# Performance work log

Measured on AMD Instinct MI355X. Metric: run time of the kernel, lower is better.

The kernel has to match this reference:

```python
import jax, jax.numpy as jnp
import numpy as np

BCE_W, AMP_W, SMOOTH_W = 1.0, 0.5, 0.3
BIG = 1e30  # finite sentinel for masked min/max (avoids inf-inf NaNs)


def setup_inputs() -> dict:
    key = jax.random.key(0)
    k1, k2, k3 = jax.random.split(key, 3)
    B, L = 128, 100000
    signals = jax.random.normal(k1, (B, 1, L), dtype=jnp.float32)
    predictions = jax.random.normal(k2, (B, L, 1), dtype=jnp.float32)
    targets = jax.random.uniform(k3, (B, L, 1), dtype=jnp.float32)
    return {"signals": signals, "predictions": predictions, "targets": targets}


def _window_amp(mask, s, idx, L):
    # mask: [B, L] bool; s: [B, L] signal. Amplitude of s over [min_idx, max_idx].
    lo = jnp.min(jnp.where(mask, idx, L), axis=1)    # [B]
    hi = jnp.max(jnp.where(mask, idx, -1), axis=1)   # [B]
    w = (idx[None, :] >= lo[:, None]) & (idx[None, :] <= hi[:, None])  # [B, L]
    amp = jnp.max(jnp.where(w, s, -BIG), axis=1) - jnp.min(jnp.where(w, s, BIG), axis=1)
    return amp, jnp.any(mask, axis=1)


def reference(signals, predictions, targets):
    # predictions/targets: [B, L, 1] (3D path of the torch module)
    p, t = predictions, targets
    pred_sigmoid = jax.nn.sigmoid(p)
    # BCEWithLogitsLoss (mean), numerically stable
    bce_loss = jnp.mean(jnp.maximum(p, 0.0) - p * t + jnp.log1p(jnp.exp(-jnp.abs(p))))

    B, L = signals.shape[0], signals.shape[2]
    s = signals[:, 0, :]                              # [B, L]
    idx = jnp.arange(L)

    true_amp, t_has = _window_amp(t[:, :, 0] > 0.5, s, idx, L)
    pred_amp, p_has = _window_amp(pred_sigmoid[:, :, 0] > 0.5, s, idx, L)
    valid = t_has & p_has

    d = jnp.abs(true_amp - pred_amp)
    per = jnp.where(true_amp > 1e-6, d / (true_amp + 1e-6), d)
    amp_loss = jnp.sum(jnp.where(valid, per, 0.0)) / B

    # smoothness: mean |diff(pred_sigmoid, axis=1)|; L >= 2 so never empty
    smoothness_loss = jnp.mean(jnp.abs(pred_sigmoid[:, 1:, :] - pred_sigmoid[:, :-1, :]))

    return BCE_W * bce_loss + AMP_W * amp_loss + SMOOTH_W * smoothness_loss
```

## Files before the change

kernel.cpp:

```cpp
#include <hip/hip_runtime.h>
#include <math.h>
#include <float.h>

#define BATCH 128
#define LEN   100000
#define BPR   4
#define CHUNK (LEN / BPR)
#define VPS   (CHUNK / 4)
#define T     1024
#define NFULL 6
#define TAILV (VPS - NFULL * T)
#define NG    (NFULL + 1)
#define NST   NG
#define STRE  (T * 4)
#define TAILE (TAILV * 4)
#define NSEG  (BATCH * BPR)
#define NSTR  (NSEG * NST)

struct WS {
    int*   lt_tab; int* ht_tab; int* lp_tab; int* hp_tab;
    float* bce_blk; float* sm_blk;
    float* cmin; float* cmax;
    float* wmn; float* wmx;
};

static inline WS ws_layout(void* d_ws) {
    WS w;
    w.lt_tab  = (int*)d_ws;
    w.ht_tab  = w.lt_tab + NSEG;
    w.lp_tab  = w.ht_tab + NSEG;
    w.hp_tab  = w.lp_tab + NSEG;
    w.bce_blk = (float*)(w.hp_tab + NSEG);
    w.sm_blk  = w.bce_blk + NSEG;
    w.cmin    = w.sm_blk  + NSEG;
    w.cmax    = w.cmin    + NSTR;
    w.wmn     = w.cmax    + NSTR;
    w.wmx     = w.wmn     + 2 * BATCH;
    return w;
}


__global__ __launch_bounds__(T) void k_main(
        const float* __restrict__ sig,
        const float* __restrict__ pred,
        const float* __restrict__ targ,
        int* __restrict__ lt_tab, int* __restrict__ ht_tab,
        int* __restrict__ lp_tab, int* __restrict__ hp_tab,
        float* __restrict__ bce_blk, float* __restrict__ sm_blk,
        float* __restrict__ cmin_tab, float* __restrict__ cmax_tab) {
    const int b   = blockIdx.y;
    const int blk = blockIdx.x;
    const int tid = threadIdx.x;
    const size_t row = (size_t)b * LEN;
    const float* prow = pred + row;
    const float* trow = targ + row;
    const float* srow = sig  + row;
    const int base = blk * CHUNK;
    const int w = tid >> 6, lane = tid & 63;

    __shared__ float s_stmn[16][NST], s_stmx[16][NST];
    __shared__ float s_bce[16], s_sm[16];
    __shared__ int   s_lt[16], s_ht[16], s_lp[16], s_hp[16];

    float bce = 0.0f, sm = 0.0f;
    unsigned tmask = 0u, pmask = 0u;

    #pragma unroll
    for (int k = 0; k < NG; ++k) {
        const bool act = (k < NFULL) || (tid < TAILV);
        float gmn = FLT_MAX, gmx = -FLT_MAX;
        if (act) {
            const int l0 = base + (tid + k * T) * 4;
            const float4 p4 = *reinterpret_cast<const float4*>(prow + l0);
            const float4 t4 = *reinterpret_cast<const float4*>(trow + l0);
            const float4 s4 = *reinterpret_cast<const float4*>(srow + l0);
            float sg0, sg1, sg2, sg3;
            #define ONE_ELEM(pp, tt, ss, sgv, BIT) { \
                const float ap = fabsf(pp); \
                const float ee = __expf(-ap); \
                const float zz = 1.0f + ee; \
                const float rr = __builtin_amdgcn_rcpf(zz); \
                bce += fmaxf(pp, 0.0f) - (pp) * (tt) + __logf(zz); \
                sgv = ((pp) >= 0.0f) ? rr : ee * rr; \
                tmask |= ((tt) > 0.5f) ? (1u << (BIT)) : 0u; \
                pmask |= ((pp) > 0.0f) ? (1u << (BIT)) : 0u; \
                gmn = fminf(gmn, (ss)); gmx = fmaxf(gmx, (ss)); }
            ONE_ELEM(p4.x, t4.x, s4.x, sg0, 4 * k + 0)
            ONE_ELEM(p4.y, t4.y, s4.y, sg1, 4 * k + 1)
            ONE_ELEM(p4.z, t4.z, s4.z, sg2, 4 * k + 2)
            ONE_ELEM(p4.w, t4.w, s4.w, sg3, 4 * k + 3)
            #undef ONE_ELEM
            sm += fabsf(sg1 - sg0) + fabsf(sg2 - sg1) + fabsf(sg3 - sg2);
            const float prev3 = __shfl_up(sg3, 1);
            if (lane == 0) {
                if (l0 > 0) {
                    const float pp = prow[l0 - 1];
                    const float ee = __expf(-fabsf(pp));
                    const float rr = __builtin_amdgcn_rcpf(1.0f + ee);
                    const float sp = (pp >= 0.0f) ? rr : ee * rr;
                    sm += fabsf(sg0 - sp);
                }
            } else {
                sm += fabsf(sg0 - prev3);
            }
        }
        #pragma unroll
        for (int o = 32; o > 0; o >>= 1) {
            gmn = fminf(gmn, __shfl_xor(gmn, o));
            gmx = fmaxf(gmx, __shfl_xor(gmx, o));
        }
        if (lane == 0) { s_stmn[w][k] = gmn; s_stmx[w][k] = gmx; }
    }

    int lt = LEN, ht = -1, lp = LEN, hp = -1;
    if (tmask) {
        const int f = __ffs(tmask) - 1;
        const int h = 31 - __clz((int)tmask);
        lt = base + (tid + (f >> 2) * T) * 4 + (f & 3);
        ht = base + (tid + (h >> 2) * T) * 4 + (h & 3);
    }
    if (pmask) {
        const int f = __ffs(pmask) - 1;
        const int h = 31 - __clz((int)pmask);
        lp = base + (tid + (f >> 2) * T) * 4 + (f & 3);
        hp = base + (tid + (h >> 2) * T) * 4 + (h & 3);
    }

    #pragma unroll
    for (int o = 32; o > 0; o >>= 1) {
        bce += __shfl_xor(bce, o);
        sm  += __shfl_xor(sm,  o);
        lt   = min(lt, __shfl_xor(lt, o));
        ht   = max(ht, __shfl_xor(ht, o));
        lp   = min(lp, __shfl_xor(lp, o));
        hp   = max(hp, __shfl_xor(hp, o));
    }
    if (lane == 0) {
        s_bce[w] = bce; s_sm[w] = sm;
        s_lt[w] = lt; s_ht[w] = ht; s_lp[w] = lp; s_hp[w] = hp;
    }
    __syncthreads();

    const int e = b * BPR + blk;
    if (tid == 0) {
        float B = 0.0f, S = 0.0f;
        int LT = LEN, HT = -1, LP = LEN, HP = -1;
        #pragma unroll
        for (int i = 0; i < 16; ++i) {
            B += s_bce[i]; S += s_sm[i];
            LT = min(LT, s_lt[i]); HT = max(HT, s_ht[i]);
            LP = min(LP, s_lp[i]); HP = max(HP, s_hp[i]);
        }
        bce_blk[e] = B; sm_blk[e] = S;
        lt_tab[e] = LT; ht_tab[e] = HT;
        lp_tab[e] = LP; hp_tab[e] = HP;
    }
    if (tid < NST) {
        float mn = s_stmn[0][tid], mx = s_stmx[0][tid];
        #pragma unroll
        for (int i = 1; i < 16; ++i) {
            mn = fminf(mn, s_stmn[i][tid]); mx = fmaxf(mx, s_stmx[i][tid]);
        }
        cmin_tab[e * NST + tid] = mn;
        cmax_tab[e * NST + tid] = mx;
    }
}


__device__ __forceinline__ int stripe_of(int l) {
    const int bk = l / CHUNK;
    int st = (l - bk * CHUNK) >> 12;
    return bk * NST + st;
}
__device__ __forceinline__ int stripe_start(int sid) {
    const int bk = sid / NST, st = sid - bk * NST;
    return bk * CHUNK + st * STRE;
}
__device__ __forceinline__ int stripe_end(int sid) {
    const int bk = sid / NST, st = sid - bk * NST;
    return bk * CHUNK + st * STRE + ((st < NST - 1) ? STRE : TAILE) - 1;
}

__global__ __launch_bounds__(512) void k_rows(
        const float* __restrict__ sig,
        const int* __restrict__ lt_tab, const int* __restrict__ ht_tab,
        const int* __restrict__ lp_tab, const int* __restrict__ hp_tab,
        const float* __restrict__ cmin_tab, const float* __restrict__ cmax_tab,
        float* __restrict__ wmn, float* __restrict__ wmx) {
    const int b     = blockIdx.x;
    const int which = blockIdx.y;
    const int tid   = threadIdx.x;
    const int* lo_tab = which ? lp_tab : lt_tab;
    const int* hi_tab = which ? hp_tab : ht_tab;

    int lo = LEN, hi = -1;
    if (tid < BPR) { lo = lo_tab[b * BPR + tid]; hi = hi_tab[b * BPR + tid]; }
    #pragma unroll
    for (int o = 32; o > 0; o >>= 1) {
        lo = min(lo, __shfl_xor(lo, o));
        hi = max(hi, __shfl_xor(hi, o));
    }
    __shared__ int s_lo, s_hi;
    if (tid == 0) { s_lo = lo; s_hi = hi; }
    __syncthreads();
    lo = s_lo; hi = s_hi;

    float mn = FLT_MAX, mx = -FLT_MAX;
    if (lo < LEN) {
        const float* srow = sig + (size_t)b * LEN;
        const int sl = stripe_of(lo), sh = stripe_of(hi);
        const int e1 = (sl == sh) ? hi : stripe_end(sl);
        for (int l = lo + tid; l <= e1; l += 512) {
            const float x = srow[l]; mn = fminf(mn, x); mx = fmaxf(mx, x);
        }
        if (sh > sl) {
            for (int l = stripe_start(sh) + tid; l <= hi; l += 512) {
                const float x = srow[l]; mn = fminf(mn, x); mx = fmaxf(mx, x);
            }
            const float* cmin_row = cmin_tab + b * BPR * NST;
            const float* cmax_row = cmax_tab + b * BPR * NST;
            for (int s = sl + 1 + tid; s < sh; s += 512) {
                mn = fminf(mn, cmin_row[s]); mx = fmaxf(mx, cmax_row[s]);
            }
        }
    }
    #pragma unroll
    for (int o = 32; o > 0; o >>= 1) {
        mn = fminf(mn, __shfl_xor(mn, o));
        mx = fmaxf(mx, __shfl_xor(mx, o));
    }
    __shared__ float sh_mn[8], sh_mx[8];
    const int w = tid >> 6, lane = tid & 63;
    if (lane == 0) { sh_mn[w] = mn; sh_mx[w] = mx; }
    __syncthreads();
    if (tid == 0) {
        float MN = FLT_MAX, MX = -FLT_MAX;
        #pragma unroll
        for (int i = 0; i < 8; ++i) {
            MN = fminf(MN, sh_mn[i]); MX = fmaxf(MX, sh_mx[i]);
        }
        if (lo >= LEN) { MN = 1e30f; MX = -1e30f; }
        wmn[which * BATCH + b] = MN;
        wmx[which * BATCH + b] = MX;
    }
}


__global__ void k_combine(const float* __restrict__ bce_blk,
                          const float* __restrict__ sm_blk,
                          const float* __restrict__ wmn,
                          const float* __restrict__ wmx,
                          float* __restrict__ out) {
    const int tid = threadIdx.x;
    float acc_b = 0.0f, acc_s = 0.0f, acc_a = 0.0f;
    for (int i = tid; i < NSEG; i += 256) { acc_b += bce_blk[i]; acc_s += sm_blk[i]; }
    if (tid < BATCH) {
        const float tmn = wmn[tid],          tmx = wmx[tid];
        const float pmn = wmn[BATCH + tid],  pmx = wmx[BATCH + tid];
        if (tmx >= tmn && pmx >= pmn) {
            const float ta = tmx - tmn;
            const float pa = pmx - pmn;
            const float d  = fabsf(ta - pa);
            acc_a = (ta > 1e-6f) ? d / (ta + 1e-6f) : d;
        }
    }
    #pragma unroll
    for (int o = 32; o > 0; o >>= 1) {
        acc_b += __shfl_xor(acc_b, o);
        acc_s += __shfl_xor(acc_s, o);
        acc_a += __shfl_xor(acc_a, o);
    }
    __shared__ float sb[4], ss[4], sa[4];
    const int w = tid >> 6, lane = tid & 63;
    if (lane == 0) { sb[w] = acc_b; ss[w] = acc_s; sa[w] = acc_a; }
    __syncthreads();
    if (tid == 0) {
        const double B = (double)(sb[0] + sb[1] + sb[2] + sb[3]);
        const double S = (double)(ss[0] + ss[1] + ss[2] + ss[3]);
        const double A = (double)(sa[0] + sa[1] + sa[2] + sa[3]);
        const double bce = B / ((double)BATCH * (double)LEN);
        const double smo = S / ((double)BATCH * (double)(LEN - 1));
        const double amp = A / (double)BATCH;
        out[0] = (float)(1.0 * bce + 0.5 * amp + 0.3 * smo);
    }
}


extern "C" void kernel_launch(void* const* d_in, const int* in_sizes, int n_in,
                              void* d_out, int out_size, void* d_ws, size_t ws_size,
                              hipStream_t stream) {
    const float* signals = (const float*)d_in[0];
    const float* preds   = (const float*)d_in[1];
    const float* targs   = (const float*)d_in[2];
    float* out = (float*)d_out;
    WS w = ws_layout(d_ws);

    dim3 gm(BPR, BATCH);
    k_main<<<gm, T, 0, stream>>>(signals, preds, targs,
                                 w.lt_tab, w.ht_tab, w.lp_tab, w.hp_tab,
                                 w.bce_blk, w.sm_blk, w.cmin, w.cmax);

    dim3 gr(BATCH, 2);
    k_rows<<<gr, 512, 0, stream>>>(signals,
                                   w.lt_tab, w.ht_tab, w.lp_tab, w.hp_tab,
                                   w.cmin, w.cmax, w.wmn, w.wmx);

    k_combine<<<1, 256, 0, stream>>>(w.bce_blk, w.sm_blk, w.wmn, w.wmx, out);
}
```

Before: 45.93 us.

## Split rows into more blocks and keep one signal min/max per chunk

Doubles the blocks per row and halves the threads per block in the main pass. The per-stripe signal min/max tables, with their per-iteration wavefront shuffles and shared-memory staging, become a single min/max per chunk folded into the final block reduction. The row-window kernel now scans raw signal only inside the partial edge chunks and uses the per-chunk extrema for the full chunks in between. This trims reduction overhead and may spread the main pass more evenly across CUs. The trade-off is that the edge chunks are now 12500 elements instead of 4096-element stripes, so the row-window pass can read far more signal data when the window starts or ends near a chunk boundary.

Result: slower. 52.12 us (+13.5%).

```diff
diff --git a/kernel.cpp b/kernel.cpp
--- a/kernel.cpp
+++ b/kernel.cpp
@@ -4,18 +4,14 @@
 
 #define BATCH 128
 #define LEN   100000
-#define BPR   4
+#define BPR   8
 #define CHUNK (LEN / BPR)
 #define VPS   (CHUNK / 4)
-#define T     1024
+#define T     512
 #define NFULL 6
 #define TAILV (VPS - NFULL * T)
 #define NG    (NFULL + 1)
-#define NST   NG
-#define STRE  (T * 4)
-#define TAILE (TAILV * 4)
 #define NSEG  (BATCH * BPR)
-#define NSTR  (NSEG * NST)
 
 struct WS {
     int*   lt_tab; int* ht_tab; int* lp_tab; int* hp_tab;
@@ -33,8 +29,8 @@
     w.bce_blk = (float*)(w.hp_tab + NSEG);
     w.sm_blk  = w.bce_blk + NSEG;
     w.cmin    = w.sm_blk  + NSEG;
-    w.cmax    = w.cmin    + NSTR;
-    w.wmn     = w.cmax    + NSTR;
+    w.cmax    = w.cmin    + NSEG;
+    w.wmn     = w.cmax    + NSEG;
     w.wmx     = w.wmn     + 2 * BATCH;
     return w;
 }
@@ -58,17 +54,13 @@
     const int base = blk * CHUNK;
     const int w = tid >> 6, lane = tid & 63;
 
-    __shared__ float s_stmn[16][NST], s_stmx[16][NST];
-    __shared__ float s_bce[16], s_sm[16];
-    __shared__ int   s_lt[16], s_ht[16], s_lp[16], s_hp[16];
-
     float bce = 0.0f, sm = 0.0f;
+    float cmn = FLT_MAX, cmx = -FLT_MAX;
     unsigned tmask = 0u, pmask = 0u;
 
     #pragma unroll
     for (int k = 0; k < NG; ++k) {
         const bool act = (k < NFULL) || (tid < TAILV);
-        float gmn = FLT_MAX, gmx = -FLT_MAX;
         if (act) {
             const int l0 = base + (tid + k * T) * 4;
             const float4 p4 = *reinterpret_cast<const float4*>(prow + l0);
@@ -84,7 +76,7 @@
                 sgv = ((pp) >= 0.0f) ? rr : ee * rr; \
                 tmask |= ((tt) > 0.5f) ? (1u << (BIT)) : 0u; \
                 pmask |= ((pp) > 0.0f) ? (1u << (BIT)) : 0u; \
-                gmn = fminf(gmn, (ss)); gmx = fmaxf(gmx, (ss)); }
+                cmn = fminf(cmn, (ss)); cmx = fmaxf(cmx, (ss)); }
             ONE_ELEM(p4.x, t4.x, s4.x, sg0, 4 * k + 0)
             ONE_ELEM(p4.y, t4.y, s4.y, sg1, 4 * k + 1)
             ONE_ELEM(p4.z, t4.z, s4.z, sg2, 4 * k + 2)
@@ -104,12 +96,6 @@
                 sm += fabsf(sg0 - prev3);
             }
         }
-        #pragma unroll
-        for (int o = 32; o > 0; o >>= 1) {
-            gmn = fminf(gmn, __shfl_xor(gmn, o));
-            gmx = fmaxf(gmx, __shfl_xor(gmx, o));
-        }
-        if (lane == 0) { s_stmn[w][k] = gmn; s_stmx[w][k] = gmx; }
     }
 
     int lt = LEN, ht = -1, lp = LEN, hp = -1;
@@ -130,58 +116,41 @@
     for (int o = 32; o > 0; o >>= 1) {
         bce += __shfl_xor(bce, o);
         sm  += __shfl_xor(sm,  o);
+        cmn  = fminf(cmn, __shfl_xor(cmn, o));
+        cmx  = fmaxf(cmx, __shfl_xor(cmx, o));
         lt   = min(lt, __shfl_xor(lt, o));
         ht   = max(ht, __shfl_xor(ht, o));
         lp   = min(lp, __shfl_xor(lp, o));
         hp   = max(hp, __shfl_xor(hp, o));
     }
+
+    __shared__ float s_bce[8], s_sm[8], s_mn[8], s_mx[8];
+    __shared__ int   s_lt[8], s_ht[8], s_lp[8], s_hp[8];
     if (lane == 0) {
-        s_bce[w] = bce; s_sm[w] = sm;
+        s_bce[w] = bce; s_sm[w] = sm; s_mn[w] = cmn; s_mx[w] = cmx;
         s_lt[w] = lt; s_ht[w] = ht; s_lp[w] = lp; s_hp[w] = hp;
     }
     __syncthreads();
-
-    const int e = b * BPR + blk;
     if (tid == 0) {
-        float B = 0.0f, S = 0.0f;
+        float B = 0.0f, S = 0.0f, MN = FLT_MAX, MX = -FLT_MAX;
         int LT = LEN, HT = -1, LP = LEN, HP = -1;
         #pragma unroll
-        for (int i = 0; i < 16; ++i) {
+        for (int i = 0; i < 8; ++i) {
             B += s_bce[i]; S += s_sm[i];
+            MN = fminf(MN, s_mn[i]); MX = fmaxf(MX, s_mx[i]);
             LT = min(LT, s_lt[i]); HT = max(HT, s_ht[i]);
             LP = min(LP, s_lp[i]); HP = max(HP, s_hp[i]);
         }
+        const int e = b * BPR + blk;
         bce_blk[e] = B; sm_blk[e] = S;
+        cmin_tab[e] = MN; cmax_tab[e] = MX;
         lt_tab[e] = LT; ht_tab[e] = HT;
         lp_tab[e] = LP; hp_tab[e] = HP;
     }
-    if (tid < NST) {
-        float mn = s_stmn[0][tid], mx = s_stmx[0][tid];
-        #pragma unroll
-        for (int i = 1; i < 16; ++i) {
-            mn = fminf(mn, s_stmn[i][tid]); mx = fmaxf(mx, s_stmx[i][tid]);
-        }
-        cmin_tab[e * NST + tid] = mn;
-        cmax_tab[e * NST + tid] = mx;
-    }
-}
-
-
-__device__ __forceinline__ int stripe_of(int l) {
-    const int bk = l / CHUNK;
-    int st = (l - bk * CHUNK) >> 12;
-    return bk * NST + st;
-}
-__device__ __forceinline__ int stripe_start(int sid) {
-    const int bk = sid / NST, st = sid - bk * NST;
-    return bk * CHUNK + st * STRE;
-}
-__device__ __forceinline__ int stripe_end(int sid) {
-    const int bk = sid / NST, st = sid - bk * NST;
-    return bk * CHUNK + st * STRE + ((st < NST - 1) ? STRE : TAILE) - 1;
-}
-
-__global__ __launch_bounds__(512) void k_rows(
+}
+
+
+__global__ __launch_bounds__(T) void k_rows(
         const float* __restrict__ sig,
         const int* __restrict__ lt_tab, const int* __restrict__ ht_tab,
         const int* __restrict__ lp_tab, const int* __restrict__ hp_tab,
@@ -208,19 +177,19 @@
     float mn = FLT_MAX, mx = -FLT_MAX;
     if (lo < LEN) {
         const float* srow = sig + (size_t)b * LEN;
-        const int sl = stripe_of(lo), sh = stripe_of(hi);
-        const int e1 = (sl == sh) ? hi : stripe_end(sl);
-        for (int l = lo + tid; l <= e1; l += 512) {
+        const int cl = lo / CHUNK, ch = hi / CHUNK;
+        const int e1 = (cl == ch) ? hi : cl * CHUNK + CHUNK - 1;
+        for (int l = lo + tid; l <= e1; l += T) {
             const float x = srow[l]; mn = fminf(mn, x); mx = fmaxf(mx, x);
         }
-        if (sh > sl) {
-            for (int l = stripe_start(sh) + tid; l <= hi; l += 512) {
+        if (ch > cl) {
+            for (int l = ch * CHUNK + tid; l <= hi; l += T) {
                 const float x = srow[l]; mn = fminf(mn, x); mx = fmaxf(mx, x);
             }
-            const float* cmin_row = cmin_tab + b * BPR * NST;
-            const float* cmax_row = cmax_tab + b * BPR * NST;
-            for (int s = sl + 1 + tid; s < sh; s += 512) {
-                mn = fminf(mn, cmin_row[s]); mx = fmaxf(mx, cmax_row[s]);
+            const float* cmin_row = cmin_tab + b * BPR;
+            const float* cmax_row = cmax_tab + b * BPR;
+            for (int c = cl + 1 + tid; c < ch; c += T) {
+                mn = fminf(mn, cmin_row[c]); mx = fmaxf(mx, cmax_row[c]);
             }
         }
     }
@@ -301,9 +270,9 @@
                                  w.bce_blk, w.sm_blk, w.cmin, w.cmax);
 
     dim3 gr(BATCH, 2);
-    k_rows<<<gr, 512, 0, stream>>>(signals,
-                                   w.lt_tab, w.ht_tab, w.lp_tab, w.hp_tab,
-                                   w.cmin, w.cmax, w.wmn, w.wmx);
+    k_rows<<<gr, T, 0, stream>>>(signals,
+                                 w.lt_tab, w.ht_tab, w.lp_tab, w.hp_tab,
+                                 w.cmin, w.cmax, w.wmn, w.wmx);
 
     k_combine<<<1, 256, 0, stream>>>(w.bce_blk, w.sm_blk, w.wmn, w.wmx, out);
 }
```
